# Optimization experiments

Measured on AMD Instinct MI355X. Metric: run time of the kernel, lower is better.

Reference implementation:

```python
import jax, jax.numpy as jnp
import numpy as np

ITERATIONS = 20  # Resonator(iterations=20)
B, F, V, D = 128, 4, 2048, 4096


def _hardsign(x):
    # bipolar normalization used by MAP-VSA multiset(normalize=True); ties -> +1
    return jnp.where(x >= 0, 1.0, -1.0).astype(x.dtype)


def setup_inputs() -> dict:
    key = jax.random.key(0)
    k1, k2 = jax.random.split(key, 2)
    # bipolar codebooks: (F, V, D)
    codebooks = _hardsign(jax.random.normal(k1, (F, V, D), dtype=jnp.float32))
    # a realistic composite input: bind (elementwise product) of one codevector per factor
    idx = jax.random.randint(k2, (B, F), 0, V)                       # (B, F)
    chosen = codebooks[jnp.arange(F)[None, :], idx]                  # (B, F, D)
    inputs = jnp.prod(chosen, axis=1)                                # (B, D)
    # standard resonator init: normalized superposition of each codebook
    init_estimates = jnp.broadcast_to(
        _hardsign(jnp.sum(codebooks, axis=1)), (B, F, D)
    ).astype(jnp.float32)                                            # (B, F, D)
    return {"inputs": inputs, "init_estimates": init_estimates, "codebooks": codebooks}


def _resonator_step(inputs, est, codebooks):
    # est: (B, F, D). rolled stack over k=1..F-1 -> (B, F, F-1, D)
    f = est.shape[-2]
    rolled = jnp.stack([jnp.roll(est, k, axis=-2) for k in range(1, f)], axis=-2)
    inv_others = jnp.prod(rolled, axis=-2)          # multibind over dim -2 -> (B, F, D)
    new_est = inputs[:, None, :] * inv_others       # bind -> (B, F, D)
    sim = jnp.einsum('bfd,fvd->bfv', new_est, codebooks)   # similarity (activation='NONE')
    # multiset(codebooks, sim, normalize=True)
    return _hardsign(jnp.einsum('bfv,fvd->bfd', sim, codebooks))


def reference(inputs, init_estimates, codebooks):
    def body(carry, i):
        est, k, done = carry
        new = _resonator_step(inputs, est, codebooks)
        eq = jnp.all(new == est)          # convergence check (fixed point)
        k = jnp.where(done, k, i)
        return (new, k, done | eq), None

    carry0 = (init_estimates, jnp.int32(0), jnp.bool_(False))
    (est, k, _), _ = jax.lax.scan(body, carry0, jnp.arange(ITERATIONS, dtype=jnp.int32))
    # cleanup: argmax of |similarity| per factor (argmax_abs=True)
    sim = jnp.einsum('bfd,fvd->bfv', est, codebooks)
    outcome = jnp.argmax(jnp.abs(sim), axis=-1)     # (B, F) int indices
    return outcome, k
```

## Files before the change

### kernel.cpp

```cpp
#include <hip/hip_runtime.h>
#include <hip/hip_bf16.h>
#include <stdint.h>

#define B_    128
#define F_    4
#define V_    2048
#define D_    4096
#define DW    64
#define VW    32
#define ITERS 20
#define NKT   16

typedef _Float16 half8 __attribute__((ext_vector_type(8)));
typedef float   floatx4 __attribute__((ext_vector_type(4)));

__global__ __launch_bounds__(256) void k_pack(const float* __restrict__ x,
                                              uint64_t* __restrict__ bits, int n) {
    int t = blockIdx.x * blockDim.x + threadIdx.x;
    if (t * 16 >= n) return;
    const float4* p = (const float4*)x + (size_t)t * 4;
    uint32_t m = 0;
    #pragma unroll
    for (int j = 0; j < 4; ++j) {
        float4 v = p[j];
        m |= (__float_as_uint(v.x) >> 31) << (4 * j + 0);
        m |= (__float_as_uint(v.y) >> 31) << (4 * j + 1);
        m |= (__float_as_uint(v.z) >> 31) << (4 * j + 2);
        m |= (__float_as_uint(v.w) >> 31) << (4 * j + 3);
    }
    ((unsigned short*)bits)[t] = (unsigned short)m;
}

__global__ void k_packT(const uint64_t* __restrict__ cb_bits,
                        uint64_t* __restrict__ cbT) {
    int vw = blockIdx.x, dwg = blockIdx.y, f = blockIdx.z;
    int lane = threadIdx.x & 63;
    int dw = dwg * 4 + (threadIdx.x >> 6);
    uint64_t w = cb_bits[((size_t)f * V_ + vw * 64 + lane) * DW + dw];
    uint64_t r = 0;
    for (int d2 = 0; d2 < 64; ++d2) {
        uint64_t m = __ballot((unsigned)((w >> d2) & 1));
        if (lane == d2) r = m;
    }
    cbT[((size_t)f * D_ + dw * 64 + lane) * VW + vw] = r;
}

__global__ __launch_bounds__(256) void k_sim(
        const uint64_t* __restrict__ cb_bits,
        const uint64_t* __restrict__ in_bits,
        const uint64_t* __restrict__ est_bits,
        _Float16* __restrict__ simf,
        const int* __restrict__ flags, int iter) {
    if (iter > 0 && flags[iter - 1] == 0) return;
    int vt = blockIdx.x, bt = blockIdx.y, f = blockIdx.z;
    int tid = threadIdx.x;
    __shared__ __align__(16) uint64_t nb[4][DW];
    {
        int bl = tid >> 6, w = tid & 63;
        int b = bt * 4 + bl;
        const uint64_t* e = est_bits + (size_t)b * F_ * DW;
        nb[bl][w] = in_bits[(size_t)b * DW + w] ^ e[0 * DW + w] ^ e[1 * DW + w]
                  ^ e[2 * DW + w] ^ e[3 * DW + w] ^ e[(size_t)f * DW + w];
    }
    __syncthreads();
    int v = vt * 256 + tid;
    int acc[4];
    #pragma unroll
    for (int bl = 0; bl < 4; ++bl) acc[bl] = 2048;
    const uint64_t* cbrow = cb_bits + ((size_t)f * V_ + v) * DW;
    #pragma unroll 2
    for (int w = 0; w < DW; w += 4) {
        ulonglong4 c4 = *(const ulonglong4*)&cbrow[w];
        #pragma unroll
        for (int bl = 0; bl < 4; ++bl) {
            const uint64_t* nrow = &nb[bl][w];
            acc[bl] -= __popcll(nrow[0] ^ c4.x) + __popcll(nrow[1] ^ c4.y)
                     + __popcll(nrow[2] ^ c4.z) + __popcll(nrow[3] ^ c4.w);
        }
    }
    #pragma unroll
    for (int bl = 0; bl < 4; ++bl)
        simf[((size_t)f * B_ + bt * 4 + bl) * V_ + v] = (_Float16)acc[bl];
}

__global__ __launch_bounds__(256) void k_gemm(
        const _Float16* __restrict__ simf,
        const uint64_t* __restrict__ cbT,
        uint64_t* __restrict__ est_bits,
        int* __restrict__ flags, int iter) {
    if (iter > 0 && flags[iter - 1] == 0) return;
    int nt = blockIdx.x, mt = blockIdx.y, f = blockIdx.z;
    int m0 = mt * 64, n0 = nt * 64;
    int tid = threadIdx.x;
    int lane = tid & 63, wave = tid >> 6;
    int lrow = lane & 15, lq = lane >> 4;
    int wm = wave & 1, wn = wave >> 1;

    __shared__ __align__(16) uint64_t Bb[64 * VW];
    __shared__ __align__(16) _Float16 As[64 * 128];
    __shared__ int bd;
    if (tid == 0) bd = 0;

    const uint64_t* bsrc = cbT + ((size_t)f * D_ + n0) * VW;
    #pragma unroll
    for (int p = 0; p < 4; ++p) {
        int chunk = p * 256 + tid;
        int dloc = chunk >> 4, cw = chunk & 15;
        ulonglong2 val = *(const ulonglong2*)&bsrc[dloc * VW + cw * 2];
        *(ulonglong2*)&Bb[dloc * VW + ((cw ^ (dloc & 15)) * 2)] = val;
    }

    const _Float16* Ab = simf + (size_t)f * B_ * V_ + (size_t)m0 * V_;
    int arow = tid >> 4, acol = tid & 15;
    half8 areg[4];
    #pragma unroll
    for (int p = 0; p < 4; ++p)
        areg[p] = *(const half8*)&Ab[(size_t)(p * 16 + arow) * V_ + acol * 8];

    floatx4 acc[2][2] = {};

    const uint64_t SPREAD = 0x1000200040008000ull;
    const uint64_t SMASK  = 0x8000800080008000ull;
    const uint64_t PONE   = 0x3C003C003C003C00ull;

    #pragma unroll 1
    for (int kt = 0; kt < NKT; ++kt) {
        __syncthreads();
        #pragma unroll
        for (int p = 0; p < 4; ++p)
            *(half8*)&As[(p * 16 + arow) * 128 + ((acol ^ arow) * 8)] = areg[p];
        if (kt + 1 < NKT) {
            #pragma unroll
            for (int p = 0; p < 4; ++p)
                areg[p] = *(const half8*)&Ab[(size_t)(p * 16 + arow) * V_ + (kt + 1) * 128 + acol * 8];
        }
        __syncthreads();

        ulonglong2 bw[2];
        #pragma unroll
        for (int nt2 = 0; nt2 < 2; ++nt2) {
            int dloc = wn * 32 + nt2 * 16 + lrow;
            bw[nt2] = *(const ulonglong2*)&Bb[dloc * VW + ((kt ^ (dloc & 15)) * 2)];
        }
        #pragma unroll
        for (int ks = 0; ks < 4; ++ks) {
            half8 af[2];
            #pragma unroll
            for (int mt2 = 0; mt2 < 2; ++mt2) {
                int row = wm * 32 + mt2 * 16 + lrow;
                af[mt2] = *(const half8*)&As[row * 128 + (((ks * 4 + lq) ^ lrow) * 8)];
            }
            half8 bfrag[2];
            #pragma unroll
            for (int nt2 = 0; nt2 < 2; ++nt2) {
                uint64_t w = (ks < 2) ? bw[nt2].x : bw[nt2].y;
                uint32_t byte = (uint32_t)(w >> ((((ks & 1) * 4 + lq)) * 8)) & 0xFFu;
                union { uint64_t q[2]; half8 h; } bu;
                bu.q[0] = (((uint64_t)(byte & 0xFu) * SPREAD) & SMASK) ^ PONE;
                bu.q[1] = (((uint64_t)(byte >> 4)   * SPREAD) & SMASK) ^ PONE;
                bfrag[nt2] = bu.h;
            }
            #pragma unroll
            for (int mt2 = 0; mt2 < 2; ++mt2)
                #pragma unroll
                for (int nt2 = 0; nt2 < 2; ++nt2)
                    acc[mt2][nt2] = __builtin_amdgcn_mfma_f32_16x16x32_f16(
                        af[mt2], bfrag[nt2], acc[mt2][nt2], 0, 0, 0);
        }
    }

    __syncthreads();
    unsigned char* S = (unsigned char*)As;
    #pragma unroll
    for (int mt2 = 0; mt2 < 2; ++mt2)
        #pragma unroll
        for (int nt2 = 0; nt2 < 2; ++nt2)
            #pragma unroll
            for (int r = 0; r < 4; ++r) {
                int row = wm * 32 + mt2 * 16 + lq * 4 + r;
                int col = wn * 32 + nt2 * 16 + lrow;
                S[row * 64 + col] = (acc[mt2][nt2][r] < 0.0f) ? 1 : 0;
            }
    __syncthreads();
    if (tid < 64) {
        const uint64_t* Sw = (const uint64_t*)S;
        uint64_t m = 0;
        #pragma unroll
        for (int j = 0; j < 8; ++j) {
            uint64_t w = Sw[tid * 8 + j];
            m |= ((w * 0x0102040810204080ull) >> 56) << (8 * j);
        }
        size_t widx = ((size_t)(m0 + tid) * F_ + f) * DW + nt;
        uint64_t old = est_bits[widx];
        est_bits[widx] = m;
        if (old != m) atomicOr(&bd, 1);
    }
    __syncthreads();
    if (tid == 0 && bd) atomicOr(&flags[iter], 1);
}

__global__ __launch_bounds__(256) void k_argmax(
        const uint64_t* __restrict__ cb_bits,
        const uint64_t* __restrict__ est_bits,
        int* __restrict__ keys) {
    int vt = blockIdx.x, bg = blockIdx.y, f = blockIdx.z;
    int tid = threadIdx.x, lane = tid & 63;
    __shared__ __align__(16) uint64_t eb[16][DW];
    #pragma unroll
    for (int j = 0; j < 4; ++j) {
        int idx = tid + j * 256;
        int bl = idx >> 6, w = idx & 63;
        eb[bl][w] = est_bits[((size_t)(bg * 16 + bl) * F_ + f) * DW + w];
    }
    __syncthreads();
    int v = vt * 256 + tid;
    const uint64_t* cbrow = cb_bits + ((size_t)f * V_ + v) * DW;
    int pc[16];
    #pragma unroll
    for (int bl = 0; bl < 16; ++bl) pc[bl] = 0;
    for (int w = 0; w < DW; w += 2) {
        ulonglong2 c2 = *(const ulonglong2*)&cbrow[w];
        #pragma unroll
        for (int bl = 0; bl < 16; ++bl) {
            ulonglong2 e2 = *(const ulonglong2*)&eb[bl][w];
            pc[bl] += __popcll(e2.x ^ c2.x) + __popcll(e2.y ^ c2.y);
        }
    }
    int key[16];
    #pragma unroll
    for (int bl = 0; bl < 16; ++bl) {
        int m = 2048 - pc[bl]; if (m < 0) m = -m;
        key[bl] = (m << 11) | (2047 - v);
    }
    #pragma unroll
    for (int s = 1; s < 64; s <<= 1)
        #pragma unroll
        for (int bl = 0; bl < 16; ++bl) {
            int o = __shfl_xor(key[bl], s, 64);
            if (o > key[bl]) key[bl] = o;
        }
    if (lane == 0)
        for (int bl = 0; bl < 16; ++bl)
            atomicMax(&keys[(size_t)(bg * 16 + bl) * F_ + f], key[bl]);
}

__global__ void k_final(const int* __restrict__ keys, const int* __restrict__ flags,
                        int* __restrict__ out) {
    int tid = blockIdx.x * blockDim.x + threadIdx.x;
    if (tid < B_ * F_) out[tid] = 2047 - (keys[tid] & 0x7FF);
    if (tid == 0) {
        int k = ITERS - 1;
        for (int i = 0; i < ITERS; ++i) if (flags[i] == 0) { k = i; break; }
        out[B_ * F_] = k;
    }
}

extern "C" void kernel_launch(void* const* d_in, const int* in_sizes, int n_in,
                              void* d_out, int out_size, void* d_ws, size_t ws_size,
                              hipStream_t stream) {
    const float* inputs = (const float*)d_in[0];
    const float* inite  = (const float*)d_in[1];
    const float* cb     = (const float*)d_in[2];
    int* out = (int*)d_out;

    char* ws = (char*)d_ws;
    uint64_t* cb_bits  = (uint64_t*)ws;  ws += (size_t)F_ * V_ * DW * 8;
    uint64_t* cbT_bits = (uint64_t*)ws;  ws += (size_t)F_ * D_ * VW * 8;
    uint64_t* est_bits = (uint64_t*)ws;  ws += (size_t)B_ * F_ * DW * 8;
    uint64_t* in_bits  = (uint64_t*)ws;  ws += (size_t)B_ * DW * 8;
    _Float16* simf     = (_Float16*)ws;  ws += (size_t)F_ * B_ * V_ * 2;
    int*      flags    = (int*)ws;       ws += 32 * 4;
    int*      keys     = (int*)ws;       ws += B_ * F_ * 4;

    hipMemsetAsync(flags, 0, (32 + B_ * F_) * sizeof(int), stream);
    k_pack<<<(F_ * V_ * D_) / 4096, 256, 0, stream>>>(cb,     cb_bits,  F_ * V_ * D_);
    k_pack<<<(B_ * F_ * D_) / 4096, 256, 0, stream>>>(inite,  est_bits, B_ * F_ * D_);
    k_pack<<<(B_ * D_) / 4096,      256, 0, stream>>>(inputs, in_bits,  B_ * D_);
    k_packT<<<dim3(32, 16, 4), 256, 0, stream>>>(cb_bits, cbT_bits);

    for (int i = 0; i < ITERS; ++i) {
        k_sim<<<dim3(8, 32, 4), 256, 0, stream>>>(cb_bits, in_bits, est_bits, simf, flags, i);
        k_gemm<<<dim3(64, 2, 4), 256, 0, stream>>>(simf, cbT_bits, est_bits, flags, i);
    }
    k_argmax<<<dim3(8, 8, 4), 256, 0, stream>>>(cb_bits, est_bits, keys);
    k_final<<<2, 256, 0, stream>>>(keys, flags, out);
}
```

Measured before the change: 1.051 ms.

## Register-tile binary popcount similarity and argmax with swizzled shared-memory staging

Rewrites the XOR-popcount similarity kernel so each block stages a 64x64 tile of codebook rows and bound-estimate rows in XOR-swizzled shared memory. Each thread then computes a 4x4 register tile of popcounts, replacing the old pattern where every thread streamed a full codebook row from global memory for only 4 batch rows. The final argmax kernel is restructured the same way: it stages all 128 estimates plus 32 codebook rows, computes an 8x2 tile per thread and reduces with 16-lane shuffles before the atomics. The aim is much higher data reuse per global load, at the cost of more shared-memory traffic and fewer, larger blocks (256 for sim, 256 for argmax).

```diff
diff --git a/kernel.cpp b/kernel.cpp
--- a/kernel.cpp
+++ b/kernel.cpp
@@ -53,34 +53,73 @@
         const int* __restrict__ flags, int iter) {
     if (iter > 0 && flags[iter - 1] == 0) return;
     int vt = blockIdx.x, bt = blockIdx.y, f = blockIdx.z;
+    int v0 = vt * 64, b0 = bt * 64;
     int tid = threadIdx.x;
-    __shared__ __align__(16) uint64_t nb[4][DW];
-    {
-        int bl = tid >> 6, w = tid & 63;
-        int b = bt * 4 + bl;
-        const uint64_t* e = est_bits + (size_t)b * F_ * DW;
-        nb[bl][w] = in_bits[(size_t)b * DW + w] ^ e[0 * DW + w] ^ e[1 * DW + w]
-                  ^ e[2 * DW + w] ^ e[3 * DW + w] ^ e[(size_t)f * DW + w];
-    }
-    __syncthreads();
-    int v = vt * 256 + tid;
-    int acc[4];
-    #pragma unroll
-    for (int bl = 0; bl < 4; ++bl) acc[bl] = 2048;
-    const uint64_t* cbrow = cb_bits + ((size_t)f * V_ + v) * DW;
-    #pragma unroll 2
-    for (int w = 0; w < DW; w += 4) {
-        ulonglong4 c4 = *(const ulonglong4*)&cbrow[w];
-        #pragma unroll
-        for (int bl = 0; bl < 4; ++bl) {
-            const uint64_t* nrow = &nb[bl][w];
-            acc[bl] -= __popcll(nrow[0] ^ c4.x) + __popcll(nrow[1] ^ c4.y)
-                     + __popcll(nrow[2] ^ c4.z) + __popcll(nrow[3] ^ c4.w);
-        }
-    }
-    #pragma unroll
-    for (int bl = 0; bl < 4; ++bl)
-        simf[((size_t)f * B_ + bt * 4 + bl) * V_ + v] = (_Float16)acc[bl];
+
+    __shared__ __align__(16) ulonglong2 CB2[64 * 32];
+    __shared__ __align__(16) ulonglong2 NB2[64 * 32];
+
+    #pragma unroll
+    for (int it = 0; it < 8; ++it) {
+        int cq = it * 256 + tid;
+        int r = cq >> 5, ch = cq & 31;
+        const ulonglong2* src = (const ulonglong2*)(cb_bits + ((size_t)f * V_ + v0 + r) * DW);
+        CB2[r * 32 + (ch ^ (r & 7))] = src[ch];
+    }
+    #pragma unroll
+    for (int it = 0; it < 8; ++it) {
+        int cq = it * 256 + tid;
+        int r = cq >> 5, ch = cq & 31;
+        int b = b0 + r;
+        const ulonglong2* iv = (const ulonglong2*)(in_bits + (size_t)b * DW);
+        const uint64_t* eb = est_bits + (size_t)b * F_ * DW;
+        ulonglong2 i2 = iv[ch];
+        ulonglong2 e0 = ((const ulonglong2*)(eb + 0 * DW))[ch];
+        ulonglong2 e1 = ((const ulonglong2*)(eb + 1 * DW))[ch];
+        ulonglong2 e2 = ((const ulonglong2*)(eb + 2 * DW))[ch];
+        ulonglong2 e3 = ((const ulonglong2*)(eb + 3 * DW))[ch];
+        ulonglong2 es = e0;
+        if (f == 1) es = e1; else if (f == 2) es = e2; else if (f == 3) es = e3;
+        ulonglong2 val;
+        val.x = i2.x ^ e0.x ^ e1.x ^ e2.x ^ e3.x ^ es.x;
+        val.y = i2.y ^ e0.y ^ e1.y ^ e2.y ^ e3.y ^ es.y;
+        NB2[r * 32 + (ch ^ (r & 7))] = val;
+    }
+    __syncthreads();
+
+    int vv = tid & 15, bb = tid >> 4;
+    int svz = vv & 7, sbz = bb & 7;
+    int pc[4][4];
+    #pragma unroll
+    for (int j = 0; j < 4; ++j)
+        #pragma unroll
+        for (int i = 0; i < 4; ++i) pc[j][i] = 0;
+
+    #pragma unroll 4
+    for (int ch = 0; ch < 32; ++ch) {
+        ulonglong2 c[4], n[4];
+        #pragma unroll
+        for (int i = 0; i < 4; ++i)
+            c[i] = CB2[(vv + 16 * i) * 32 + (ch ^ svz)];
+        #pragma unroll
+        for (int j = 0; j < 4; ++j)
+            n[j] = NB2[(bb + 16 * j) * 32 + (ch ^ sbz)];
+        #pragma unroll
+        for (int j = 0; j < 4; ++j)
+            #pragma unroll
+            for (int i = 0; i < 4; ++i)
+                pc[j][i] += __popcll(n[j].x ^ c[i].x) + __popcll(n[j].y ^ c[i].y);
+    }
+
+    #pragma unroll
+    for (int j = 0; j < 4; ++j) {
+        int b = b0 + bb + 16 * j;
+        #pragma unroll
+        for (int i = 0; i < 4; ++i) {
+            int v = v0 + vv + 16 * i;
+            simf[((size_t)f * B_ + b) * V_ + v] = (_Float16)(2048 - pc[j][i]);
+        }
+    }
 }
 
 __global__ __launch_bounds__(256) void k_gemm(
@@ -203,45 +242,69 @@
         const uint64_t* __restrict__ cb_bits,
         const uint64_t* __restrict__ est_bits,
         int* __restrict__ keys) {
-    int vt = blockIdx.x, bg = blockIdx.y, f = blockIdx.z;
-    int tid = threadIdx.x, lane = tid & 63;
-    __shared__ __align__(16) uint64_t eb[16][DW];
-    #pragma unroll
-    for (int j = 0; j < 4; ++j) {
-        int idx = tid + j * 256;
-        int bl = idx >> 6, w = idx & 63;
-        eb[bl][w] = est_bits[((size_t)(bg * 16 + bl) * F_ + f) * DW + w];
-    }
-    __syncthreads();
-    int v = vt * 256 + tid;
-    const uint64_t* cbrow = cb_bits + ((size_t)f * V_ + v) * DW;
-    int pc[16];
-    #pragma unroll
-    for (int bl = 0; bl < 16; ++bl) pc[bl] = 0;
-    for (int w = 0; w < DW; w += 2) {
-        ulonglong2 c2 = *(const ulonglong2*)&cbrow[w];
-        #pragma unroll
-        for (int bl = 0; bl < 16; ++bl) {
-            ulonglong2 e2 = *(const ulonglong2*)&eb[bl][w];
-            pc[bl] += __popcll(e2.x ^ c2.x) + __popcll(e2.y ^ c2.y);
-        }
-    }
-    int key[16];
-    #pragma unroll
-    for (int bl = 0; bl < 16; ++bl) {
-        int m = 2048 - pc[bl]; if (m < 0) m = -m;
-        key[bl] = (m << 11) | (2047 - v);
-    }
-    #pragma unroll
-    for (int s = 1; s < 64; s <<= 1)
-        #pragma unroll
-        for (int bl = 0; bl < 16; ++bl) {
-            int o = __shfl_xor(key[bl], s, 64);
-            if (o > key[bl]) key[bl] = o;
-        }
-    if (lane == 0)
-        for (int bl = 0; bl < 16; ++bl)
-            atomicMax(&keys[(size_t)(bg * 16 + bl) * F_ + f], key[bl]);
+    int vt = blockIdx.x, f = blockIdx.y;
+    int v0 = vt * 32;
+    int tid = threadIdx.x;
+
+    __shared__ __align__(16) ulonglong2 EB2[128 * 32];
+    __shared__ __align__(16) ulonglong2 CBa[32 * 32];
+
+    #pragma unroll
+    for (int it = 0; it < 16; ++it) {
+        int cq = it * 256 + tid;
+        int r = cq >> 5, ch = cq & 31;
+        const ulonglong2* src = (const ulonglong2*)(est_bits + ((size_t)r * F_ + f) * DW);
+        EB2[r * 32 + (ch ^ (r & 7))] = src[ch];
+    }
+    #pragma unroll
+    for (int it = 0; it < 4; ++it) {
+        int cq = it * 256 + tid;
+        int r = cq >> 5, ch = cq & 31;
+        const ulonglong2* src = (const ulonglong2*)(cb_bits + ((size_t)f * V_ + v0 + r) * DW);
+        CBa[r * 32 + (ch ^ (r & 7))] = src[ch];
+    }
+    __syncthreads();
+
+    int vv = tid & 15, bb = tid >> 4;
+    int svz = vv & 7, sbz = bb & 7;
+    int pc[8][2];
+    #pragma unroll
+    for (int j = 0; j < 8; ++j) { pc[j][0] = 0; pc[j][1] = 0; }
+
+    #pragma unroll 4
+    for (int ch = 0; ch < 32; ++ch) {
+        ulonglong2 c[2], n[8];
+        #pragma unroll
+        for (int i = 0; i < 2; ++i)
+            c[i] = CBa[(vv + 16 * i) * 32 + (ch ^ svz)];
+        #pragma unroll
+        for (int j = 0; j < 8; ++j)
+            n[j] = EB2[(bb + 16 * j) * 32 + (ch ^ sbz)];
+        #pragma unroll
+        for (int j = 0; j < 8; ++j)
+            #pragma unroll
+            for (int i = 0; i < 2; ++i)
+                pc[j][i] += __popcll(n[j].x ^ c[i].x) + __popcll(n[j].y ^ c[i].y);
+    }
+
+    #pragma unroll
+    for (int j = 0; j < 8; ++j) {
+        int kj = 0x80000000;
+        #pragma unroll
+        for (int i = 0; i < 2; ++i) {
+            int v = v0 + vv + 16 * i;
+            int m = 2048 - pc[j][i]; if (m < 0) m = -m;
+            int key = (m << 11) | (2047 - v);
+            if (key > kj) kj = key;
+        }
+        #pragma unroll
+        for (int s = 1; s < 16; s <<= 1) {
+            int o = __shfl_xor(kj, s, 64);
+            if (o > kj) kj = o;
+        }
+        if ((tid & 15) == 0)
+            atomicMax(&keys[(size_t)(bb + 16 * j) * F_ + f], kj);
+    }
 }
 
 __global__ void k_final(const int* __restrict__ keys, const int* __restrict__ flags,
@@ -279,9 +342,9 @@
     k_packT<<<dim3(32, 16, 4), 256, 0, stream>>>(cb_bits, cbT_bits);
 
     for (int i = 0; i < ITERS; ++i) {
-        k_sim<<<dim3(8, 32, 4), 256, 0, stream>>>(cb_bits, in_bits, est_bits, simf, flags, i);
+        k_sim<<<dim3(32, 2, 4), 256, 0, stream>>>(cb_bits, in_bits, est_bits, simf, flags, i);
         k_gemm<<<dim3(64, 2, 4), 256, 0, stream>>>(simf, cbT_bits, est_bits, flags, i);
     }
-    k_argmax<<<dim3(8, 8, 4), 256, 0, stream>>>(cb_bits, est_bits, keys);
+    k_argmax<<<dim3(64, 4), 256, 0, stream>>>(cb_bits, est_bits, keys);
     k_final<<<2, 256, 0, stream>>>(keys, flags, out);
 }
```

Measured after the change: 1.005 ms. -4.4%, faster.
